# Kernel optimization log

Hardware: AMD Instinct MI355X
Metric: run time of the kernel (lower is better)

Reference implementation:

```python
import jax, jax.numpy as jnp
import numpy as np
import math

B, S, HID = 16, 512, 768
NUM_LABELS = 9
NUM_HEADS = 4
HEAD_DIM = HID // NUM_HEADS
MAX_REL = 5
B_PERSON = 1
I_PERSON = 2
LN_EPS = 1e-5


def setup_inputs() -> dict:
    key = jax.random.key(0)
    ks = jax.random.split(key, 16)
    w = lambda k, shp: jax.random.normal(k, shp, dtype=jnp.float32) * 0.02
    return {
        "sequence_output": jax.random.normal(ks[0], (B, S, HID), dtype=jnp.float32),
        "Wq": w(ks[1], (HID, HID)), "bq": jnp.zeros((HID,), jnp.float32),
        "Wk": w(ks[2], (HID, HID)), "bk": jnp.zeros((HID,), jnp.float32),
        "Wv": w(ks[3], (HID, HID)), "bv": jnp.zeros((HID,), jnp.float32),
        "Wo": w(ks[4], (HID, HID)), "bo": jnp.zeros((HID,), jnp.float32),
        "ln_g": jnp.ones((HID,), jnp.float32), "ln_b": jnp.zeros((HID,), jnp.float32),
        "Ws": w(ks[5], (HID, NUM_LABELS)), "bs": jnp.zeros((NUM_LABELS,), jnp.float32),
        "entity_bias": w(ks[6], (NUM_LABELS,)),
    }


def _heads(x):
    # [B,S,HID] -> [B,H,S,D]
    return x.reshape(B, S, NUM_HEADS, HEAD_DIM).transpose(0, 2, 1, 3)


def reference(sequence_output, Wq, bq, Wk, bk, Wv, bv, Wo, bo, ln_g, ln_b, Ws, bs, entity_bias):
    x = sequence_output
    q = _heads(x @ Wq + bq)
    k = _heads(x @ Wk + bk)
    v = _heads(x @ Wv + bv)

    scores = jnp.einsum("bhqd,bhkd->bhqk", q, k)
    # relative position bias: exp(-0.1 * clamp(|i-j|, 0, MAX_REL)), broadcast over b,h
    idx = jnp.arange(S, dtype=jnp.float32)
    dist = jnp.abs(idx[None, :] - idx[:, None])  # [S,S]
    rel_bias = jnp.exp(-0.1 * jnp.clip(dist, 0.0, float(MAX_REL)))
    dist_mask = -0.1 * dist
    scores = (scores + rel_bias) / math.sqrt(HEAD_DIM) + dist_mask
    probs = jax.nn.softmax(scores, axis=-1)  # dropout is identity in eval

    ctx = jnp.einsum("bhqk,bhkd->bhqd", probs, v)
    ctx = ctx.transpose(0, 2, 1, 3).reshape(B, S, HID)
    out = ctx @ Wo + bo

    h = x + out
    mu = jnp.mean(h, axis=-1, keepdims=True)
    var = jnp.mean(jnp.square(h - mu), axis=-1, keepdims=True)
    h = (h - mu) * jax.lax.rsqrt(var + LN_EPS) * ln_g + ln_b

    span_logits = h @ Ws + bs  # [B,S,L]
    # vectorized entity-bias post-process: the torch loop adds entity_bias[I_PERSON]
    # TWICE to final_logits[:, j, I_PERSON] whenever argmax(span_logits[:, j-1]) == B_PERSON
    prev_is_b = jnp.argmax(span_logits[:, :-1], axis=-1) == B_PERSON  # [B,S-1]
    bump = jnp.where(prev_is_b, 2.0 * entity_bias[I_PERSON], 0.0)
    final_logits = span_logits.at[:, 1:, I_PERSON].add(bump)
    return final_logits
```

## Files before the change

kernel.cpp:

```cpp
#include <hip/hip_runtime.h>
#include <math.h>

#define SEQ 512
#define HID 768
#define NBATCH 16
#define ROWS 8192
#define INV_SQRT_D 0.07216878364870323f

typedef short s8v __attribute__((ext_vector_type(8)));
typedef _Float16 h8v __attribute__((ext_vector_type(8)));
typedef float f4v __attribute__((ext_vector_type(4)));
typedef unsigned short u16;

__device__ __forceinline__ u16 f2h(float f) {
  _Float16 h = (_Float16)f;
  return __builtin_bit_cast(u16, h);
}

__device__ __forceinline__ void llds16(const u16* g, u16* l) {
  __builtin_amdgcn_global_load_lds(
      (const __attribute__((address_space(1))) void*)g,
      (__attribute__((address_space(3))) void*)l, 16, 0, 0);
}

template <int KSTEPS>
__device__ __forceinline__ void mm_core128(
    const u16* __restrict__ A, const int lda,
    const u16* __restrict__ B, const int ldb,
    u16* lds, f4v (&acc)[4][4])
{
  const int tid = threadIdx.x;
  const int w = tid >> 6, ln = tid & 63;
  const u16* src = (w >> 1) ? B : A;
  const int ld = (w >> 1) ? ldb : lda;
  const int half = w & 1;
  const int srow = ln >> 2;
  const int csw  = ((ln & 3) - (ln >> 3)) & 3;
  const int ml = ln & 15;
  const int fo2 = (((ln >> 4) + ((ln >> 1) & 3)) & 3) * 8;
  const int wr = (w >> 1) * 64, wc = (w & 1) * 64;

  const u16* gp[4];
  u16* lp[4];
#pragma unroll
  for (int t = 0; t < 4; ++t) {
    const int row = half * 64 + t * 16 + srow;
    gp[t] = src + (size_t)row * ld + csw * 8;
    lp[t] = lds + (w >> 1) * 4096 + half * 2048 + t * 512;
  }

  for (int kp = 0; kp < KSTEPS / 2; ++kp) {
    const int k0 = kp * 64;
    __syncthreads();
#pragma unroll
    for (int t = 0; t < 4; ++t) {
      llds16(gp[t] + k0,      lp[t]);
      llds16(gp[t] + k0 + 32, lp[t] + 8192);
    }
    __syncthreads();
#pragma unroll
    for (int sub = 0; sub < 2; ++sub) {
      const int so = sub * 8192;
      h8v a[4], b[4];
#pragma unroll
      for (int i = 0; i < 4; ++i)
        a[i] = *(const h8v*)&lds[so + (wr + i * 16 + ml) * 32 + fo2];
#pragma unroll
      for (int j = 0; j < 4; ++j)
        b[j] = *(const h8v*)&lds[so + 4096 + (wc + j * 16 + ml) * 32 + fo2];
#pragma unroll
      for (int i = 0; i < 4; ++i)
#pragma unroll
        for (int j = 0; j < 4; ++j)
          acc[i][j] = __builtin_amdgcn_mfma_f32_16x16x32_f16(a[i], b[j], acc[i][j], 0, 0, 0);
    }
  }
}

__global__ __launch_bounds__(256) void splitx(const float* __restrict__ x,
                                              u16* __restrict__ xh)
{
  const int i = blockIdx.x * 256 + threadIdx.x;
  const float4 v = ((const float4*)x)[i];
  ((ushort4*)xh)[i] = make_ushort4(f2h(v.x), f2h(v.y), f2h(v.z), f2h(v.w));
}

__global__ __launch_bounds__(256) void wsplit(
    const float* __restrict__ Wq, const float* __restrict__ Wk,
    const float* __restrict__ Wv, const float* __restrict__ Wo,
    u16* __restrict__ WTh)
{
  __shared__ float t[32][33];
  const int z = blockIdx.z;
  const float* W = (z == 0) ? Wq : (z == 1) ? Wk : (z == 2) ? Wv : Wo;
  const int n0 = blockIdx.x * 32, k0 = blockIdx.y * 32;
  const int tx = threadIdx.x & 31, ty = threadIdx.x >> 5;
#pragma unroll
  for (int i = 0; i < 4; ++i)
    t[ty + 8 * i][tx] = W[(size_t)(k0 + ty + 8 * i) * HID + n0 + tx];
  __syncthreads();
#pragma unroll
  for (int i = 0; i < 4; ++i) {
    const float v = t[tx][ty + 8 * i];
    const size_t idx = (size_t)z * HID * HID + (size_t)(n0 + ty + 8 * i) * HID + k0 + tx;
    WTh[idx] = f2h(v);
  }
}

__global__ __launch_bounds__(256, 3) void qkv_mm(
    const u16* __restrict__ xh, const u16* __restrict__ WTh,
    const float* __restrict__ bq, const float* __restrict__ bk, const float* __restrict__ bv,
    u16* __restrict__ qh, u16* __restrict__ kh, u16* __restrict__ vTh)
{
  __shared__ u16 lds[16384];
  const int id = blockIdx.x;
  const int xcd = id & 7;
  const int s = id >> 3;
  const int bx = s % 6;
  const int yl = (s / 6) & 7;
  const int z  = s / 48;
  const int bm = (yl * 8 + xcd) * 128;
  const int bn = bx * 128;
  const size_t wtoff = (size_t)z * HID * HID + (size_t)bn * HID;
  f4v acc[4][4];
#pragma unroll
  for (int i = 0; i < 4; ++i)
#pragma unroll
    for (int j = 0; j < 4; ++j) acc[i][j] = (f4v)0.f;
  mm_core128<24>(xh + (size_t)bm * HID, HID, WTh + wtoff, HID, lds, acc);
  const int tid = threadIdx.x, w = tid >> 6, ln = tid & 63;
  const int ml = ln & 15, quad = ln >> 4;
  const int wr = (w >> 1) * 64, wc = (w & 1) * 64;
  if (z == 2) {
    u16* vb = vTh + (size_t)(bm >> 9) * HID * SEQ;
    const int spbase = (bm & 511) + wr + quad * 4;
#pragma unroll
    for (int i = 0; i < 4; ++i)
#pragma unroll
      for (int j = 0; j < 4; ++j) {
        const int gcol = bn + wc + j * 16 + ml;
        const float bv_ = bv[gcol];
        const ushort4 pk = make_ushort4(
            f2h(acc[i][j][0] + bv_), f2h(acc[i][j][1] + bv_),
            f2h(acc[i][j][2] + bv_), f2h(acc[i][j][3] + bv_));
        *(ushort4*)&vb[(size_t)gcol * SEQ + spbase + i * 16] = pk;
      }
  } else {
    const float* bias = (z == 0) ? bq : bk;
    u16* dst = (z == 0) ? qh : kh;
#pragma unroll
    for (int i = 0; i < 4; ++i)
#pragma unroll
      for (int j = 0; j < 4; ++j) {
        const int gcol = bn + wc + j * 16 + ml;
        const float bv_ = bias[gcol];
#pragma unroll
        for (int r = 0; r < 4; ++r) {
          const int grow = bm + wr + i * 16 + quad * 4 + r;
          dst[(size_t)grow * HID + gcol] = f2h(acc[i][j][r] + bv_);
        }
      }
  }
}

__global__ __launch_bounds__(256, 2) void attn_fused(
    const u16* __restrict__ qh, const u16* __restrict__ kh,
    const u16* __restrict__ vTh, u16* __restrict__ ch)
{
  __shared__ u16 lds[28928];
  __shared__ float gtab[1024];
  __shared__ float red[4][32];
  const int f = blockIdx.x;
  const int xcd = f & 7, s = f >> 3;
  const int z = xcd * 8 + (s >> 4);
  const int bm = (s & 15) * 32;
  const int b = z >> 2, hh = z & 3;
  const int tid = threadIdx.x, w = tid >> 6, ln = tid & 63;
  const int ml = ln & 15, quad = ln >> 4;

  for (int t = tid; t < 1023; t += 256) {
    const float fd = fabsf((float)(t - 511));
    gtab[t] = INV_SQRT_D * __expf(-0.1f * fminf(fd, 5.0f)) - 0.1f * fd;
  }

  const u16* qbase = qh + (size_t)(b * SEQ + bm) * HID + hh * 192;
  const u16* kbase = kh + (size_t)b * SEQ * HID + hh * 192;
  const u16* vbase = vTh + (size_t)b * HID * SEQ + (size_t)(hh * 192) * SEQ;

  h8v qf[2][6];
#pragma unroll
  for (int i = 0; i < 2; ++i)
#pragma unroll
    for (int ks = 0; ks < 6; ++ks)
      qf[i][ks] = *(const h8v*)(qbase + (size_t)(i * 16 + ml) * HID + ks * 32 + quad * 8);

  int koff[6], kldso[6], voff[6], vldso[6];
#pragma unroll
  for (int c = 0; c < 6; ++c) {
    const int cc = c * 256 + tid;
    const int krow = cc / 24, kcol = cc % 24;
    koff[c]  = krow * HID + kcol * 8;
    kldso[c] = krow * 200 + kcol * 8;
    const int vrow = cc >> 3, vcol = cc & 7;
    voff[c]  = vrow * SEQ + vcol * 8;
    vldso[c] = 12800 + vrow * 72 + vcol * 8;
  }
  s8v kc[6], vc[6];
#pragma unroll
  for (int c = 0; c < 6; ++c) {
    kc[c] = *(const s8v*)(kbase + koff[c]);
    vc[c] = *(const s8v*)(vbase + voff[c]);
  }

  f4v acc2[2][3];
#pragma unroll
  for (int i = 0; i < 2; ++i)
#pragma unroll
    for (int jj = 0; jj < 3; ++jj) acc2[i][jj] = (f4v)0.f;
  float rsum[2][4];
#pragma unroll
  for (int i = 0; i < 2; ++i)
#pragma unroll
    for (int r = 0; r < 4; ++r) rsum[i][r] = 0.f;

  for (int j = 0; j < 8; ++j) {
    __syncthreads();
#pragma unroll
    for (int c = 0; c < 6; ++c) {
      *(s8v*)&lds[kldso[c]] = kc[c];
      *(s8v*)&lds[vldso[c]] = vc[c];
    }
    __syncthreads();
    if (j < 7) {
      const int ko = (j + 1) * 64;
#pragma unroll
      for (int c = 0; c < 6; ++c) {
        kc[c] = *(const s8v*)(kbase + (size_t)ko * HID + koff[c]);
        vc[c] = *(const s8v*)(vbase + ko + voff[c]);
      }
    }
    f4v sacc[2];
    sacc[0] = (f4v)0.f; sacc[1] = (f4v)0.f;
    __builtin_amdgcn_s_setprio(1);
#pragma unroll
    for (int ks = 0; ks < 6; ++ks) {
      const h8v kf = *(const h8v*)&lds[(w * 16 + ml) * 200 + ks * 32 + quad * 8];
      sacc[0] = __builtin_amdgcn_mfma_f32_16x16x32_f16(qf[0][ks], kf, sacc[0], 0, 0, 0);
      sacc[1] = __builtin_amdgcn_mfma_f32_16x16x32_f16(qf[1][ks], kf, sacc[1], 0, 0, 0);
    }
    __builtin_amdgcn_s_setprio(0);
    const int scolg = j * 64 + w * 16 + ml;
#pragma unroll
    for (int i = 0; i < 2; ++i)
#pragma unroll
      for (int r = 0; r < 4; ++r) {
        const int lrow = i * 16 + quad * 4 + r;
        const float g = gtab[bm + lrow - scolg + 511];
        const float p = __expf(fmaf(sacc[i][r], INV_SQRT_D, g));
        rsum[i][r] += p;
        lds[26624 + lrow * 72 + w * 16 + ml] = f2h(p);
      }
    __syncthreads();
    __builtin_amdgcn_s_setprio(1);
#pragma unroll
    for (int ks = 0; ks < 2; ++ks) {
      h8v pf[2], vf[3];
#pragma unroll
      for (int i = 0; i < 2; ++i)
        pf[i] = *(const h8v*)&lds[26624 + (i * 16 + ml) * 72 + ks * 32 + quad * 8];
#pragma unroll
      for (int jj = 0; jj < 3; ++jj)
        vf[jj] = *(const h8v*)&lds[12800 + (w * 48 + jj * 16 + ml) * 72 + ks * 32 + quad * 8];
#pragma unroll
      for (int i = 0; i < 2; ++i)
#pragma unroll
        for (int jj = 0; jj < 3; ++jj)
          acc2[i][jj] = __builtin_amdgcn_mfma_f32_16x16x32_f16(pf[i], vf[jj], acc2[i][jj], 0, 0, 0);
    }
    __builtin_amdgcn_s_setprio(0);
  }

#pragma unroll
  for (int i = 0; i < 2; ++i)
#pragma unroll
    for (int r = 0; r < 4; ++r) {
      float t = rsum[i][r];
#pragma unroll
      for (int o = 1; o < 16; o <<= 1) t += __shfl_xor(t, o, 64);
      rsum[i][r] = t;
    }
  if (ml == 0) {
#pragma unroll
    for (int i = 0; i < 2; ++i)
#pragma unroll
      for (int r = 0; r < 4; ++r) red[w][i * 16 + quad * 4 + r] = rsum[i][r];
  }
  __syncthreads();

#pragma unroll
  for (int i = 0; i < 2; ++i)
#pragma unroll
    for (int r = 0; r < 4; ++r) {
      const int R = i * 16 + quad * 4 + r;
      const float is = 1.0f / (red[0][R] + red[1][R] + red[2][R] + red[3][R]);
      const int m = bm + R;
#pragma unroll
      for (int jj = 0; jj < 3; ++jj) {
        const int gcol = hh * 192 + w * 48 + jj * 16 + ml;
        ch[(size_t)(b * SEQ + m) * HID + gcol] = f2h(acc2[i][jj][r] * is);
      }
    }
}

__global__ __launch_bounds__(256, 3) void proj_mm(
    const u16* __restrict__ ch, const u16* __restrict__ WTh,
    const float* __restrict__ bo, const float* __restrict__ x, float* __restrict__ h)
{
  __shared__ u16 lds[16384];
  const int id = blockIdx.x;
  const int xcd = id & 7;
  const int s = id >> 3;
  const int bx = s % 6;
  const int yl = s / 6;
  const int bm = (yl * 8 + xcd) * 128;
  const int bn = bx * 128;
  const size_t wtoff = (size_t)3 * HID * HID + (size_t)bn * HID;
  f4v acc[4][4];
#pragma unroll
  for (int i = 0; i < 4; ++i)
#pragma unroll
    for (int j = 0; j < 4; ++j) acc[i][j] = (f4v)0.f;
  mm_core128<24>(ch + (size_t)bm * HID, HID, WTh + wtoff, HID, lds, acc);
  const int tid = threadIdx.x, w = tid >> 6, ln = tid & 63;
  const int ml = ln & 15, quad = ln >> 4;
  const int wr = (w >> 1) * 64, wc = (w & 1) * 64;
#pragma unroll
  for (int i = 0; i < 4; ++i)
#pragma unroll
    for (int j = 0; j < 4; ++j) {
      const int gcol = bn + wc + j * 16 + ml;
      const float bv_ = bo[gcol];
#pragma unroll
      for (int r = 0; r < 4; ++r) {
        const int grow = bm + wr + i * 16 + quad * 4 + r;
        const size_t idx = (size_t)grow * HID + gcol;
        h[idx] = acc[i][j][r] + bv_ + x[idx];
      }
    }
}

__global__ __launch_bounds__(256) void ln_logits_kernel(
    const float* __restrict__ h, const float* __restrict__ g,
    const float* __restrict__ bta, const float* __restrict__ Ws,
    const float* __restrict__ bsv, float* __restrict__ span)
{
  const int row = blockIdx.x;
  const int tid = threadIdx.x;
  const float* hr = h + (size_t)row * HID;
  const float x0 = hr[tid], x1 = hr[tid + 256], x2 = hr[tid + 512];
  float s = x0 + x1 + x2;
  float sq = x0 * x0 + x1 * x1 + x2 * x2;
#pragma unroll
  for (int o = 32; o > 0; o >>= 1) { s += __shfl_down(s, o, 64); sq += __shfl_down(sq, o, 64); }
  __shared__ float red[8];
  __shared__ float smu, srs;
  const int wid = tid >> 6, lid = tid & 63;
  if (lid == 0) { red[wid] = s; red[4 + wid] = sq; }
  __syncthreads();
  if (tid == 0) {
    const float ts = red[0] + red[1] + red[2] + red[3];
    const float tq = red[4] + red[5] + red[6] + red[7];
    const float mu = ts / 768.0f;
    const float var = tq / 768.0f - mu * mu;
    smu = mu; srs = rsqrtf(var + 1e-5f);
  }
  __syncthreads();
  const float mu = smu, rs = srs;
  const float n0 = (x0 - mu) * rs * g[tid] + bta[tid];
  const float n1 = (x1 - mu) * rs * g[tid + 256] + bta[tid + 256];
  const float n2 = (x2 - mu) * rs * g[tid + 512] + bta[tid + 512];
  float pl[9];
#pragma unroll
  for (int l = 0; l < 9; ++l)
    pl[l] = n0 * Ws[(size_t)tid * 9 + l]
          + n1 * Ws[(size_t)(tid + 256) * 9 + l]
          + n2 * Ws[(size_t)(tid + 512) * 9 + l];
#pragma unroll
  for (int l = 0; l < 9; ++l)
#pragma unroll
    for (int o = 32; o > 0; o >>= 1) pl[l] += __shfl_down(pl[l], o, 64);
  __shared__ float lred[4][9];
  if (lid == 0) {
#pragma unroll
    for (int l = 0; l < 9; ++l) lred[wid][l] = pl[l];
  }
  __syncthreads();
  if (tid < 9) {
    span[(size_t)row * 9 + tid] =
        lred[0][tid] + lred[1][tid] + lred[2][tid] + lred[3][tid] + bsv[tid];
  }
}

__global__ __launch_bounds__(256) void bump_kernel(
    const float* __restrict__ span, const float* __restrict__ eb, float* __restrict__ out)
{
  const int idx = blockIdx.x * 256 + threadIdx.x;
  if (idx >= ROWS) return;
  const int j = idx & (SEQ - 1);
  const float* sl = span + (size_t)idx * 9;
  float v[9];
#pragma unroll
  for (int l = 0; l < 9; ++l) v[l] = sl[l];
  if (j >= 1) {
    const float* sp = sl - 9;
    float m = sp[0]; int am = 0;
#pragma unroll
    for (int l = 1; l < 9; ++l) { const float t = sp[l]; if (t > m) { m = t; am = l; } }
    if (am == 1) v[2] += 2.0f * eb[2];
  }
#pragma unroll
  for (int l = 0; l < 9; ++l) out[(size_t)idx * 9 + l] = v[l];
}

extern "C" void kernel_launch(void* const* d_in, const int* in_sizes, int n_in,
                              void* d_out, int out_size, void* d_ws, size_t ws_size,
                              hipStream_t stream)
{
  (void)in_sizes; (void)n_in; (void)out_size; (void)ws_size;
  const float* x   = (const float*)d_in[0];
  const float* Wq  = (const float*)d_in[1];
  const float* bq  = (const float*)d_in[2];
  const float* Wk  = (const float*)d_in[3];
  const float* bk  = (const float*)d_in[4];
  const float* Wv  = (const float*)d_in[5];
  const float* bv  = (const float*)d_in[6];
  const float* Wo  = (const float*)d_in[7];
  const float* bo  = (const float*)d_in[8];
  const float* lng = (const float*)d_in[9];
  const float* lnb = (const float*)d_in[10];
  const float* Ws  = (const float*)d_in[11];
  const float* bs  = (const float*)d_in[12];
  const float* eb  = (const float*)d_in[13];
  float* out = (float*)d_out;

  char* ws = (char*)d_ws;
  u16* xh  = (u16*)(ws + 0);
  u16* WTh = (u16*)(ws + 25165824);
  u16* qh  = (u16*)(ws + 34603008);
  u16* kh  = (u16*)(ws + 59768832);
  u16* vTh = (u16*)(ws + 84934656);
  float* hb = (float*)(ws + 84934656);
  float* spanb = (float*)(ws + 152043520);
  u16* ctxh = qh;

  splitx<<<dim3(1572864 / 256), 256, 0, stream>>>(x, xh);
  wsplit<<<dim3(24, 24, 4), 256, 0, stream>>>(Wq, Wk, Wv, Wo, WTh);
  qkv_mm<<<dim3(1152), 256, 0, stream>>>(xh, WTh, bq, bk, bv, qh, kh, vTh);
  attn_fused<<<dim3(1024), 256, 0, stream>>>(qh, kh, vTh, ctxh);
  proj_mm<<<dim3(384), 256, 0, stream>>>(ctxh, WTh, bo, x, hb);
  ln_logits_kernel<<<dim3(ROWS), 256, 0, stream>>>(hb, lng, lnb, Ws, bs, spanb);
  bump_kernel<<<dim3(ROWS / 256), 256, 0, stream>>>(spanb, eb, out);
}
```

Measured before the change: 226.8 us.

## Enlarge attention query tile to 64 rows and stage V-transpose stores through LDS

```diff
diff --git a/kernel.cpp b/kernel.cpp
--- a/kernel.cpp
+++ b/kernel.cpp
@@ -112,7 +112,7 @@
     const float* __restrict__ bq, const float* __restrict__ bk, const float* __restrict__ bv,
     u16* __restrict__ qh, u16* __restrict__ kh, u16* __restrict__ vTh)
 {
-  __shared__ u16 lds[16384];
+  __shared__ u16 lds[17408];
   const int id = blockIdx.x;
   const int xcd = id & 7;
   const int s = id >> 3;
@@ -132,19 +132,29 @@
   const int ml = ln & 15, quad = ln >> 4;
   const int wr = (w >> 1) * 64, wc = (w & 1) * 64;
   if (z == 2) {
+    __syncthreads();
+#pragma unroll
+    for (int i = 0; i < 4; ++i)
+#pragma unroll
+      for (int j = 0; j < 4; ++j) {
+        const int ncol = wc + j * 16 + ml;
+        const float bv_ = bv[bn + ncol];
+#pragma unroll
+        for (int r = 0; r < 4; ++r) {
+          const int srow = wr + i * 16 + quad * 4 + r;
+          lds[ncol * 136 + srow] = f2h(acc[i][j][r] + bv_);
+        }
+      }
+    __syncthreads();
     u16* vb = vTh + (size_t)(bm >> 9) * HID * SEQ;
-    const int spbase = (bm & 511) + wr + quad * 4;
-#pragma unroll
-    for (int i = 0; i < 4; ++i)
-#pragma unroll
-      for (int j = 0; j < 4; ++j) {
-        const int gcol = bn + wc + j * 16 + ml;
-        const float bv_ = bv[gcol];
-        const ushort4 pk = make_ushort4(
-            f2h(acc[i][j][0] + bv_), f2h(acc[i][j][1] + bv_),
-            f2h(acc[i][j][2] + bv_), f2h(acc[i][j][3] + bv_));
-        *(ushort4*)&vb[(size_t)gcol * SEQ + spbase + i * 16] = pk;
-      }
+    const int sq0 = bm & 511;
+    const int c8 = (tid & 15) * 8;
+#pragma unroll
+    for (int p = 0; p < 8; ++p) {
+      const int nl = p * 16 + (tid >> 4);
+      const s8v val = *(const s8v*)&lds[nl * 136 + c8];
+      *(s8v*)&vb[(size_t)(bn + nl) * SEQ + sq0 + c8] = val;
+    }
   } else {
     const float* bias = (z == 0) ? bq : bk;
     u16* dst = (z == 0) ? qh : kh;
@@ -167,23 +177,24 @@
     const u16* __restrict__ qh, const u16* __restrict__ kh,
     const u16* __restrict__ vTh, u16* __restrict__ ch)
 {
-  __shared__ u16 lds[28928];
+  __shared__ u16 lds[31232];
   __shared__ float gtab[1024];
   __shared__ float red[4][32];
   const int f = blockIdx.x;
   const int xcd = f & 7, s = f >> 3;
-  const int z = xcd * 8 + (s >> 4);
-  const int bm = (s & 15) * 32;
+  const int z = xcd * 8 + (s >> 3);
+  const int bm = (s & 7) * 64;
   const int b = z >> 2, hh = z & 3;
   const int tid = threadIdx.x, w = tid >> 6, ln = tid & 63;
   const int ml = ln & 15, quad = ln >> 4;
+  const int rh = w >> 1, ch2 = w & 1;
 
   for (int t = tid; t < 1023; t += 256) {
     const float fd = fabsf((float)(t - 511));
     gtab[t] = INV_SQRT_D * __expf(-0.1f * fminf(fd, 5.0f)) - 0.1f * fd;
   }
 
-  const u16* qbase = qh + (size_t)(b * SEQ + bm) * HID + hh * 192;
+  const u16* qbase = qh + (size_t)(b * SEQ + bm + rh * 32) * HID + hh * 192;
   const u16* kbase = kh + (size_t)b * SEQ * HID + hh * 192;
   const u16* vbase = vTh + (size_t)b * HID * SEQ + (size_t)(hh * 192) * SEQ;
 
@@ -212,11 +223,11 @@
     vc[c] = *(const s8v*)(vbase + voff[c]);
   }
 
-  f4v acc2[2][3];
+  f4v acc2[2][6];
 #pragma unroll
   for (int i = 0; i < 2; ++i)
 #pragma unroll
-    for (int jj = 0; jj < 3; ++jj) acc2[i][jj] = (f4v)0.f;
+    for (int jj = 0; jj < 6; ++jj) acc2[i][jj] = (f4v)0.f;
   float rsum[2][4];
 #pragma unroll
   for (int i = 0; i < 2; ++i)
@@ -239,42 +250,50 @@
         vc[c] = *(const s8v*)(vbase + ko + voff[c]);
       }
     }
-    f4v sacc[2];
-    sacc[0] = (f4v)0.f; sacc[1] = (f4v)0.f;
+    f4v sacc[2][2];
+    sacc[0][0] = (f4v)0.f; sacc[0][1] = (f4v)0.f;
+    sacc[1][0] = (f4v)0.f; sacc[1][1] = (f4v)0.f;
     __builtin_amdgcn_s_setprio(1);
 #pragma unroll
     for (int ks = 0; ks < 6; ++ks) {
-      const h8v kf = *(const h8v*)&lds[(w * 16 + ml) * 200 + ks * 32 + quad * 8];
-      sacc[0] = __builtin_amdgcn_mfma_f32_16x16x32_f16(qf[0][ks], kf, sacc[0], 0, 0, 0);
-      sacc[1] = __builtin_amdgcn_mfma_f32_16x16x32_f16(qf[1][ks], kf, sacc[1], 0, 0, 0);
+      h8v kf0 = *(const h8v*)&lds[(ch2 * 32 + ml) * 200 + ks * 32 + quad * 8];
+      h8v kf1 = *(const h8v*)&lds[(ch2 * 32 + 16 + ml) * 200 + ks * 32 + quad * 8];
+      sacc[0][0] = __builtin_amdgcn_mfma_f32_16x16x32_f16(qf[0][ks], kf0, sacc[0][0], 0, 0, 0);
+      sacc[1][0] = __builtin_amdgcn_mfma_f32_16x16x32_f16(qf[1][ks], kf0, sacc[1][0], 0, 0, 0);
+      sacc[0][1] = __builtin_amdgcn_mfma_f32_16x16x32_f16(qf[0][ks], kf1, sacc[0][1], 0, 0, 0);
+      sacc[1][1] = __builtin_amdgcn_mfma_f32_16x16x32_f16(qf[1][ks], kf1, sacc[1][1], 0, 0, 0);
     }
     __builtin_amdgcn_s_setprio(0);
-    const int scolg = j * 64 + w * 16 + ml;
 #pragma unroll
     for (int i = 0; i < 2; ++i)
 #pragma unroll
-      for (int r = 0; r < 4; ++r) {
-        const int lrow = i * 16 + quad * 4 + r;
-        const float g = gtab[bm + lrow - scolg + 511];
-        const float p = __expf(fmaf(sacc[i][r], INV_SQRT_D, g));
-        rsum[i][r] += p;
-        lds[26624 + lrow * 72 + w * 16 + ml] = f2h(p);
+      for (int j2 = 0; j2 < 2; ++j2) {
+        const int lcol = ch2 * 32 + j2 * 16 + ml;
+        const int scolg = j * 64 + lcol;
+#pragma unroll
+        for (int r = 0; r < 4; ++r) {
+          const int lrow = rh * 32 + i * 16 + quad * 4 + r;
+          const float g = gtab[bm + lrow - scolg + 511];
+          const float p = __expf(fmaf(sacc[i][j2][r], INV_SQRT_D, g));
+          rsum[i][r] += p;
+          lds[26624 + lrow * 72 + lcol] = f2h(p);
+        }
       }
     __syncthreads();
     __builtin_amdgcn_s_setprio(1);
 #pragma unroll
     for (int ks = 0; ks < 2; ++ks) {
-      h8v pf[2], vf[3];
+      h8v pf[2], vf[6];
 #pragma unroll
       for (int i = 0; i < 2; ++i)
-        pf[i] = *(const h8v*)&lds[26624 + (i * 16 + ml) * 72 + ks * 32 + quad * 8];
-#pragma unroll
-      for (int jj = 0; jj < 3; ++jj)
-        vf[jj] = *(const h8v*)&lds[12800 + (w * 48 + jj * 16 + ml) * 72 + ks * 32 + quad * 8];
+        pf[i] = *(const h8v*)&lds[26624 + (rh * 32 + i * 16 + ml) * 72 + ks * 32 + quad * 8];
+#pragma unroll
+      for (int jj = 0; jj < 6; ++jj)
+        vf[jj] = *(const h8v*)&lds[12800 + (ch2 * 96 + jj * 16 + ml) * 72 + ks * 32 + quad * 8];
 #pragma unroll
       for (int i = 0; i < 2; ++i)
 #pragma unroll
-        for (int jj = 0; jj < 3; ++jj)
+        for (int jj = 0; jj < 6; ++jj)
           acc2[i][jj] = __builtin_amdgcn_mfma_f32_16x16x32_f16(pf[i], vf[jj], acc2[i][jj], 0, 0, 0);
     }
     __builtin_amdgcn_s_setprio(0);
@@ -301,12 +320,12 @@
   for (int i = 0; i < 2; ++i)
 #pragma unroll
     for (int r = 0; r < 4; ++r) {
-      const int R = i * 16 + quad * 4 + r;
-      const float is = 1.0f / (red[0][R] + red[1][R] + red[2][R] + red[3][R]);
-      const int m = bm + R;
-#pragma unroll
-      for (int jj = 0; jj < 3; ++jj) {
-        const int gcol = hh * 192 + w * 48 + jj * 16 + ml;
+      const int lr = i * 16 + quad * 4 + r;
+      const float is = 1.0f / (red[rh * 2][lr] + red[rh * 2 + 1][lr]);
+      const int m = bm + rh * 32 + lr;
+#pragma unroll
+      for (int jj = 0; jj < 6; ++jj) {
+        const int gcol = hh * 192 + ch2 * 96 + jj * 16 + ml;
         ch[(size_t)(b * SEQ + m) * HID + gcol] = f2h(acc2[i][jj][r] * is);
       }
     }
@@ -456,7 +475,7 @@
   splitx<<<dim3(1572864 / 256), 256, 0, stream>>>(x, xh);
   wsplit<<<dim3(24, 24, 4), 256, 0, stream>>>(Wq, Wk, Wv, Wo, WTh);
   qkv_mm<<<dim3(1152), 256, 0, stream>>>(xh, WTh, bq, bk, bv, qh, kh, vTh);
-  attn_fused<<<dim3(1024), 256, 0, stream>>>(qh, kh, vTh, ctxh);
+  attn_fused<<<dim3(512), 256, 0, stream>>>(qh, kh, vTh, ctxh);
   proj_mm<<<dim3(384), 256, 0, stream>>>(ctxh, WTh, bo, x, hb);
   ln_logits_kernel<<<dim3(ROWS), 256, 0, stream>>>(hb, lng, lnb, Ws, bs, spanb);
   bump_kernel<<<dim3(ROWS / 256), 256, 0, stream>>>(spanb, eb, out);
```

Result: faster. 219.1 us (-3.4%).
